# Kernel optimization log

Measured on AMD Instinct MI355X. Metric: run time of the kernel, lower is better.

The kernel has to match this reference:

```python
import jax, jax.numpy as jnp
import numpy as np

B, L, D = 8, 2048, 64


def setup_inputs() -> dict:
    key = jax.random.key(0)
    kq, kk, kv = jax.random.split(key, 3)
    query = jax.random.normal(kq, (B, L, D), dtype=jnp.float32)
    key_t = jax.random.normal(kk, (B, L, D), dtype=jnp.float32)
    value = jax.random.normal(kv, (B, L, D), dtype=jnp.float32)
    return {"query": query, "key": key_t, "value": value}


def reference(query, key, value):
    d = query.shape[-1]
    # e = Q K^T / sqrt(d_k)   -> [B, Lq, Lk]
    scale = 1.0 / np.sqrt(float(d)).astype(np.float32)
    e = jnp.einsum("bqd,bkd->bqk", query, key) * scale
    # stable softmax over keys (matches exp(e - max)/sum in source)
    attention = jax.nn.softmax(e, axis=-1)
    # v = A V   -> [B, Lq, Dv]
    return jnp.einsum("bqk,bkd->bqd", attention, value)
```

## Files before the change

### kernel.cpp

```cpp
#include <hip/hip_runtime.h>


#define B_ 8
#define L_ 2048
#define D_ 64
#define NT 256

typedef _Float16 half8_t __attribute__((ext_vector_type(8)));
typedef _Float16 half4_t __attribute__((ext_vector_type(4)));
typedef float f32x4 __attribute__((ext_vector_type(4)));

#define SCALE_LOG2E 0.1803368801111244f

__global__ __launch_bounds__(NT) void prepass_frag(
    const float* __restrict__ K, const float* __restrict__ V,
    _Float16* __restrict__ K16F, _Float16* __restrict__ VT16F)
{
    const int blk = blockIdx.x;
    const int t = threadIdx.x;
    if (blk < 512) {
        const int b  = blk >> 6;
        const int kt = blk & 63;
        const int p    = t >> 6;
        const int lane = t & 63;
        const int quad = lane >> 4;
        const int l15  = lane & 15;
        const int s = p >> 1, c = p & 1;
        const int row = kt * 32 + s * 16 + l15;
        const float* kp = K + ((size_t)b * L_ + row) * D_ + c * 32 + quad * 8;
        const float4 f0 = *(const float4*)kp;
        const float4 f1 = *(const float4*)(kp + 4);
        half8_t w;
        w[0] = (_Float16)f0.x; w[1] = (_Float16)f0.y;
        w[2] = (_Float16)f0.z; w[3] = (_Float16)f0.w;
        w[4] = (_Float16)f1.x; w[5] = (_Float16)f1.y;
        w[6] = (_Float16)f1.z; w[7] = (_Float16)f1.w;
        *(half8_t*)&K16F[((size_t)(b * 64 + kt) * 4 + p) * 512 + lane * 8] = w;
    } else {
        const int vb = blk - 512;
        const int b  = vb >> 6;
        const int kt = vb & 63;
        #pragma unroll
        for (int i = 0; i < 2; ++i) {
            const int slot = i * NT + t;
            const int p    = slot >> 6;
            const int lane = slot & 63;
            const int quad = lane >> 4;
            const int l15  = lane & 15;
            const int d = p >> 1, ks = p & 1;
            const int row = kt * 32 + ks * 16 + quad * 4;
            const int col = d * 16 + l15;
            const float* vp = V + ((size_t)b * L_ + row) * D_ + col;
            half4_t a;
            a[0] = (_Float16)vp[0];
            a[1] = (_Float16)vp[D_];
            a[2] = (_Float16)vp[2 * D_];
            a[3] = (_Float16)vp[3 * D_];
            *(half4_t*)&VT16F[((size_t)(b * 64 + kt) * 8 + p) * 256 + lane * 4] = a;
        }
    }
}


#define LOADK(KT, BK)                                                           \
    {                                                                           \
        _Pragma("unroll") for (int s = 0; s < 2; ++s)                           \
        _Pragma("unroll") for (int c = 0; c < 2; ++c)                           \
            BK[s][c] = *(const half8_t*)&KbF[((size_t)(KT) * 4 + s * 2 + c) * 512 + lane * 8]; \
    }

#define PROC(KT, BK)                                                            \
    {                                                                           \
        half4_t av[4][2];                                                       \
        _Pragma("unroll") for (int d = 0; d < 4; ++d)                           \
        _Pragma("unroll") for (int ks = 0; ks < 2; ++ks)                        \
            av[d][ks] = *(const half4_t*)&VbF[((size_t)(KT) * 8 + d * 2 + ks) * 256 + lane * 4]; \
        f32x4 sc[2][2];                                                         \
        _Pragma("unroll") for (int ks = 0; ks < 2; ++ks)                        \
        _Pragma("unroll") for (int qs = 0; qs < 2; ++qs) {                      \
            f32x4 acc = (f32x4){0.f, 0.f, 0.f, 0.f};                            \
            acc = __builtin_amdgcn_mfma_f32_16x16x32_f16(BK[ks][0], bq[qs][0], acc, 0, 0, 0); \
            acc = __builtin_amdgcn_mfma_f32_16x16x32_f16(BK[ks][1], bq[qs][1], acc, 0, 0, 0); \
            sc[ks][qs] = acc;                                                   \
        }                                                                       \
        half4_t pb[2][2];                                                       \
        _Pragma("unroll") for (int ks = 0; ks < 2; ++ks)                        \
        _Pragma("unroll") for (int qs = 0; qs < 2; ++qs) {                      \
            const float p0 = __builtin_exp2f(sc[ks][qs][0]);                    \
            const float p1 = __builtin_exp2f(sc[ks][qs][1]);                    \
            const float p2 = __builtin_exp2f(sc[ks][qs][2]);                    \
            const float p3 = __builtin_exp2f(sc[ks][qs][3]);                    \
            lacc[qs] += (p0 + p1) + (p2 + p3);                                  \
            half4_t pv;                                                         \
            pv[0] = (_Float16)p0; pv[1] = (_Float16)p1;                         \
            pv[2] = (_Float16)p2; pv[3] = (_Float16)p3;                         \
            pb[ks][qs] = pv;                                                    \
        }                                                                       \
        _Pragma("unroll") for (int qs = 0; qs < 2; ++qs)                        \
        _Pragma("unroll") for (int d = 0; d < 4; ++d)                           \
        _Pragma("unroll") for (int ks = 0; ks < 2; ++ks)                        \
            ofr[qs][d] = __builtin_amdgcn_mfma_f32_16x16x16f16(av[d][ks], pb[ks][qs], ofr[qs][d], 0, 0, 0); \
    }

__global__ __launch_bounds__(512, 4) void attn_tlp(
    const float* __restrict__ Q,
    const _Float16* __restrict__ K16F,
    const _Float16* __restrict__ VT16F,
    float* __restrict__ O)
{
    __shared__ float Ored[512 * 17];
    __shared__ float Lred[256];

    const int t    = threadIdx.x;
    const int wave = t >> 6;
    const int lane = t & 63;
    const int quad = lane >> 4;
    const int l15  = lane & 15;

    const int b   = blockIdx.x & 7;
    const int qbi = blockIdx.x >> 3;
    const int qb  = qbi * 32;
    const int kt0 = wave * 8;

    const _Float16* KbF = K16F + (size_t)b * 64 * 4 * 512;
    const _Float16* VbF = VT16F + (size_t)b * 64 * 8 * 256;

    half8_t bq[2][2];
    #pragma unroll
    for (int qs = 0; qs < 2; ++qs) {
        const float* qp = Q + ((size_t)b * L_ + qb + qs * 16 + l15) * D_ + quad * 8;
        #pragma unroll
        for (int c = 0; c < 2; ++c) {
            const float4 f0 = *(const float4*)(qp + c * 32);
            const float4 f1 = *(const float4*)(qp + c * 32 + 4);
            bq[qs][c][0] = (_Float16)(f0.x * SCALE_LOG2E);
            bq[qs][c][1] = (_Float16)(f0.y * SCALE_LOG2E);
            bq[qs][c][2] = (_Float16)(f0.z * SCALE_LOG2E);
            bq[qs][c][3] = (_Float16)(f0.w * SCALE_LOG2E);
            bq[qs][c][4] = (_Float16)(f1.x * SCALE_LOG2E);
            bq[qs][c][5] = (_Float16)(f1.y * SCALE_LOG2E);
            bq[qs][c][6] = (_Float16)(f1.z * SCALE_LOG2E);
            bq[qs][c][7] = (_Float16)(f1.w * SCALE_LOG2E);
        }
    }

    f32x4 ofr[2][4];
    #pragma unroll
    for (int qs = 0; qs < 2; ++qs)
        #pragma unroll
        for (int d = 0; d < 4; ++d)
            ofr[qs][d] = (f32x4){0.f, 0.f, 0.f, 0.f};
    float lacc[2] = {0.f, 0.f};

    half8_t bkA[2][2], bkB[2][2];
    LOADK(kt0, bkA);
    for (int it = 0; it < 4; ++it) {
        const int kta = kt0 + it * 2;
        LOADK(kta + 1, bkB);
        PROC(kta, bkA);
        LOADK(kta + 2, bkA);
        PROC(kta + 1, bkB);
    }

    #pragma unroll
    for (int qs = 0; qs < 2; ++qs) {
        float v = lacc[qs];
        v += __shfl_xor(v, 16, 64);
        v += __shfl_xor(v, 32, 64);
        lacc[qs] = v;
    }
    if (quad == 0) {
        Lred[wave * 32 + l15] = lacc[0];
        Lred[wave * 32 + 16 + l15] = lacc[1];
    }

    #pragma unroll
    for (int qs = 0; qs < 2; ++qs) {
        __syncthreads();
        #pragma unroll
        for (int d = 0; d < 4; ++d)
            #pragma unroll
            for (int r = 0; r < 4; ++r)
                Ored[(wave * 64 + lane) * 17 + d * 4 + r] = ofr[qs][d][r];
        __syncthreads();
        if (wave < 4) {
            float lt = 0.f;
            #pragma unroll
            for (int w2 = 0; w2 < 8; ++w2)
                lt += Lred[w2 * 32 + qs * 16 + l15];
            const float inv = 1.0f / lt;
            f32x4 osum = (f32x4){0.f, 0.f, 0.f, 0.f};
            #pragma unroll
            for (int w2 = 0; w2 < 8; ++w2) {
                const float* src = &Ored[(w2 * 64 + lane) * 17 + wave * 4];
                osum[0] += src[0]; osum[1] += src[1];
                osum[2] += src[2]; osum[3] += src[3];
            }
            float4 outv;
            outv.x = osum[0] * inv; outv.y = osum[1] * inv;
            outv.z = osum[2] * inv; outv.w = osum[3] * inv;
            *(float4*)&O[((size_t)b * L_ + qb + qs * 16 + l15) * D_ + wave * 16 + quad * 4] = outv;
        }
    }
}

#define KS 72
__global__ __launch_bounds__(NT) void attn_mfma_f16(
    const float* __restrict__ Q, const float* __restrict__ K,
    const float* __restrict__ V, float* __restrict__ O)
{
    __shared__ __align__(16) _Float16 Kt[64 * KS];
    __shared__ __align__(16) _Float16 Vt[D_ * KS];
    __shared__ __align__(16) _Float16 Pt[4][16 * KS];

    const int t = threadIdx.x;
    const int wave = t >> 6, lane = t & 63, quad = lane >> 4, l15 = lane & 15;
    const int bpb = L_ / 64;
    const int b = blockIdx.x / bpb;
    const int qb = (blockIdx.x % bpb) * 64 + wave * 16;
    const size_t boff = (size_t)b * L_ * D_;

    half8_t aq[2];
    {
        const float* qp = Q + boff + (size_t)(qb + l15) * D_ + quad * 8;
        #pragma unroll
        for (int c = 0; c < 2; ++c) {
            const float4* p4 = (const float4*)(qp + c * 32);
            const float4 f0 = p4[0], f1 = p4[1];
            aq[c][0] = (_Float16)f0.x; aq[c][1] = (_Float16)f0.y;
            aq[c][2] = (_Float16)f0.z; aq[c][3] = (_Float16)f0.w;
            aq[c][4] = (_Float16)f1.x; aq[c][5] = (_Float16)f1.y;
            aq[c][6] = (_Float16)f1.z; aq[c][7] = (_Float16)f1.w;
        }
    }
    f32x4 ofr[4];
    #pragma unroll
    for (int d = 0; d < 4; ++d) ofr[d] = (f32x4){0.f, 0.f, 0.f, 0.f};
    float lacc[4] = {0.f, 0.f, 0.f, 0.f};
    const int skey = t & 63, sdg = t >> 6;
    _Float16* Pw = &Pt[wave][0];

    for (int kt = 0; kt < L_ / 64; ++kt) {
        __syncthreads();
        {
            const float4* kg4 = (const float4*)(K + boff + (size_t)(kt * 64 + skey) * D_ + sdg * 16);
            const float4 f0 = kg4[0], f1 = kg4[1], f2 = kg4[2], f3 = kg4[3];
            half8_t w0, w1;
            w0[0] = (_Float16)f0.x; w0[1] = (_Float16)f0.y;
            w0[2] = (_Float16)f0.z; w0[3] = (_Float16)f0.w;
            w0[4] = (_Float16)f1.x; w0[5] = (_Float16)f1.y;
            w0[6] = (_Float16)f1.z; w0[7] = (_Float16)f1.w;
            w1[0] = (_Float16)f2.x; w1[1] = (_Float16)f2.y;
            w1[2] = (_Float16)f2.z; w1[3] = (_Float16)f2.w;
            w1[4] = (_Float16)f3.x; w1[5] = (_Float16)f3.y;
            w1[6] = (_Float16)f3.z; w1[7] = (_Float16)f3.w;
            *(half8_t*)&Kt[skey * KS + sdg * 16] = w0;
            *(half8_t*)&Kt[skey * KS + sdg * 16 + 8] = w1;
        }
        {
            const float4* vg4 = (const float4*)(V + boff + (size_t)(kt * 64 + skey) * D_ + sdg * 16);
            #pragma unroll
            for (int i = 0; i < 4; ++i) {
                const float4 f = vg4[i];
                const int d0 = sdg * 16 + i * 4;
                Vt[(d0 + 0) * KS + skey] = (_Float16)f.x;
                Vt[(d0 + 1) * KS + skey] = (_Float16)f.y;
                Vt[(d0 + 2) * KS + skey] = (_Float16)f.z;
                Vt[(d0 + 3) * KS + skey] = (_Float16)f.w;
            }
        }
        __syncthreads();
        #pragma unroll
        for (int s = 0; s < 4; ++s) {
            const half8_t bk0 = *(const half8_t*)&Kt[(s * 16 + l15) * KS + quad * 8];
            const half8_t bk1 = *(const half8_t*)&Kt[(s * 16 + l15) * KS + 32 + quad * 8];
            f32x4 sc = (f32x4){0.f, 0.f, 0.f, 0.f};
            sc = __builtin_amdgcn_mfma_f32_16x16x32_f16(aq[0], bk0, sc, 0, 0, 0);
            sc = __builtin_amdgcn_mfma_f32_16x16x32_f16(aq[1], bk1, sc, 0, 0, 0);
            #pragma unroll
            for (int r = 0; r < 4; ++r) {
                const float p = __expf(sc[r] * 0.125f);
                lacc[r] += p;
                Pw[(quad * 4 + r) * KS + s * 16 + l15] = (_Float16)p;
            }
        }
        __syncthreads();
        #pragma unroll
        for (int c = 0; c < 2; ++c) {
            const half8_t ap = *(const half8_t*)&Pw[l15 * KS + c * 32 + quad * 8];
            #pragma unroll
            for (int d = 0; d < 4; ++d) {
                const half8_t bv = *(const half8_t*)&Vt[(d * 16 + l15) * KS + c * 32 + quad * 8];
                ofr[d] = __builtin_amdgcn_mfma_f32_16x16x32_f16(ap, bv, ofr[d], 0, 0, 0);
            }
        }
    }
    #pragma unroll
    for (int r = 0; r < 4; ++r) {
        float v = lacc[r];
        v += __shfl_xor(v, 1, 64);
        v += __shfl_xor(v, 2, 64);
        v += __shfl_xor(v, 4, 64);
        v += __shfl_xor(v, 8, 64);
        lacc[r] = v;
    }
    #pragma unroll
    for (int r = 0; r < 4; ++r) {
        const float inv = 1.0f / lacc[r];
        float* orow = O + boff + (size_t)(qb + quad * 4 + r) * D_ + l15;
        #pragma unroll
        for (int d = 0; d < 4; ++d) orow[d * 16] = ofr[d][r] * inv;
    }
}

extern "C" void kernel_launch(void* const* d_in, const int* in_sizes, int n_in,
                              void* d_out, int out_size, void* d_ws, size_t ws_size,
                              hipStream_t stream) {
    const float* Q = (const float*)d_in[0];
    const float* K = (const float*)d_in[1];
    const float* V = (const float*)d_in[2];
    float* O = (float*)d_out;

    if (ws_size >= (size_t)8 * 1024 * 1024) {
        _Float16* K16F  = (_Float16*)d_ws;
        _Float16* VT16F = K16F + (size_t)1048576;
        prepass_frag<<<1024, NT, 0, stream>>>(K, V, K16F, VT16F);
        attn_tlp<<<512, 512, 0, stream>>>(Q, K16F, VT16F, O);
    } else {
        attn_mfma_f16<<<256, NT, 0, stream>>>(Q, K, V, O);
    }
}
```

Baseline: 83.33 us.

## Fuse K/V fp16 conversion into attention kernel with double-buffered LDS tiles

Drops the separate prepass kernel and its global fp16 workspace. A single fused kernel now loads fp32 K/V, converts them into MFMA fragment layout in double-buffered shared memory, and prefetches the next tile from global memory while computing the current one. Each block covers 64 queries with 8 waves, split into 4 query groups by 2 key halves, and the two halves are combined through LDS at the end. This removes one launch and the workspace round trip. In exchange there are fewer blocks (256), a barrier on every tile, and each block repeats the fp32-to-fp16 conversion work.

```diff
diff --git a/kernel.cpp b/kernel.cpp
--- a/kernel.cpp
+++ b/kernel.cpp
@@ -4,7 +4,6 @@
 #define B_ 8
 #define L_ 2048
 #define D_ 64
-#define NT 256
 
 typedef _Float16 half8_t __attribute__((ext_vector_type(8)));
 typedef _Float16 half4_t __attribute__((ext_vector_type(4)));
@@ -12,304 +11,173 @@
 
 #define SCALE_LOG2E 0.1803368801111244f
 
-__global__ __launch_bounds__(NT) void prepass_frag(
-    const float* __restrict__ K, const float* __restrict__ V,
-    _Float16* __restrict__ K16F, _Float16* __restrict__ VT16F)
+__global__ __launch_bounds__(512, 2) void attn_fused(
+    const float* __restrict__ Q, const float* __restrict__ K,
+    const float* __restrict__ V, float* __restrict__ O)
 {
-    const int blk = blockIdx.x;
-    const int t = threadIdx.x;
-    if (blk < 512) {
-        const int b  = blk >> 6;
-        const int kt = blk & 63;
-        const int p    = t >> 6;
-        const int lane = t & 63;
-        const int quad = lane >> 4;
-        const int l15  = lane & 15;
-        const int s = p >> 1, c = p & 1;
-        const int row = kt * 32 + s * 16 + l15;
-        const float* kp = K + ((size_t)b * L_ + row) * D_ + c * 32 + quad * 8;
-        const float4 f0 = *(const float4*)kp;
-        const float4 f1 = *(const float4*)(kp + 4);
-        half8_t w;
-        w[0] = (_Float16)f0.x; w[1] = (_Float16)f0.y;
-        w[2] = (_Float16)f0.z; w[3] = (_Float16)f0.w;
-        w[4] = (_Float16)f1.x; w[5] = (_Float16)f1.y;
-        w[6] = (_Float16)f1.z; w[7] = (_Float16)f1.w;
-        *(half8_t*)&K16F[((size_t)(b * 64 + kt) * 4 + p) * 512 + lane * 8] = w;
-    } else {
-        const int vb = blk - 512;
-        const int b  = vb >> 6;
-        const int kt = vb & 63;
-        #pragma unroll
-        for (int i = 0; i < 2; ++i) {
-            const int slot = i * NT + t;
-            const int p    = slot >> 6;
-            const int lane = slot & 63;
-            const int quad = lane >> 4;
-            const int l15  = lane & 15;
-            const int d = p >> 1, ks = p & 1;
-            const int row = kt * 32 + ks * 16 + quad * 4;
-            const int col = d * 16 + l15;
-            const float* vp = V + ((size_t)b * L_ + row) * D_ + col;
-            half4_t a;
-            a[0] = (_Float16)vp[0];
-            a[1] = (_Float16)vp[D_];
-            a[2] = (_Float16)vp[2 * D_];
-            a[3] = (_Float16)vp[3 * D_];
-            *(half4_t*)&VT16F[((size_t)(b * 64 + kt) * 8 + p) * 256 + lane * 4] = a;
-        }
-    }
-}
-
-
-#define LOADK(KT, BK)                                                           \
-    {                                                                           \
-        _Pragma("unroll") for (int s = 0; s < 2; ++s)                           \
-        _Pragma("unroll") for (int c = 0; c < 2; ++c)                           \
-            BK[s][c] = *(const half8_t*)&KbF[((size_t)(KT) * 4 + s * 2 + c) * 512 + lane * 8]; \
-    }
-
-#define PROC(KT, BK)                                                            \
-    {                                                                           \
-        half4_t av[4][2];                                                       \
-        _Pragma("unroll") for (int d = 0; d < 4; ++d)                           \
-        _Pragma("unroll") for (int ks = 0; ks < 2; ++ks)                        \
-            av[d][ks] = *(const half4_t*)&VbF[((size_t)(KT) * 8 + d * 2 + ks) * 256 + lane * 4]; \
-        f32x4 sc[2][2];                                                         \
-        _Pragma("unroll") for (int ks = 0; ks < 2; ++ks)                        \
-        _Pragma("unroll") for (int qs = 0; qs < 2; ++qs) {                      \
-            f32x4 acc = (f32x4){0.f, 0.f, 0.f, 0.f};                            \
-            acc = __builtin_amdgcn_mfma_f32_16x16x32_f16(BK[ks][0], bq[qs][0], acc, 0, 0, 0); \
-            acc = __builtin_amdgcn_mfma_f32_16x16x32_f16(BK[ks][1], bq[qs][1], acc, 0, 0, 0); \
-            sc[ks][qs] = acc;                                                   \
-        }                                                                       \
-        half4_t pb[2][2];                                                       \
-        _Pragma("unroll") for (int ks = 0; ks < 2; ++ks)                        \
-        _Pragma("unroll") for (int qs = 0; qs < 2; ++qs) {                      \
-            const float p0 = __builtin_exp2f(sc[ks][qs][0]);                    \
-            const float p1 = __builtin_exp2f(sc[ks][qs][1]);                    \
-            const float p2 = __builtin_exp2f(sc[ks][qs][2]);                    \
-            const float p3 = __builtin_exp2f(sc[ks][qs][3]);                    \
-            lacc[qs] += (p0 + p1) + (p2 + p3);                                  \
-            half4_t pv;                                                         \
-            pv[0] = (_Float16)p0; pv[1] = (_Float16)p1;                         \
-            pv[2] = (_Float16)p2; pv[3] = (_Float16)p3;                         \
-            pb[ks][qs] = pv;                                                    \
-        }                                                                       \
-        _Pragma("unroll") for (int qs = 0; qs < 2; ++qs)                        \
-        _Pragma("unroll") for (int d = 0; d < 4; ++d)                           \
-        _Pragma("unroll") for (int ks = 0; ks < 2; ++ks)                        \
-            ofr[qs][d] = __builtin_amdgcn_mfma_f32_16x16x16f16(av[d][ks], pb[ks][qs], ofr[qs][d], 0, 0, 0); \
-    }
-
-__global__ __launch_bounds__(512, 4) void attn_tlp(
-    const float* __restrict__ Q,
-    const _Float16* __restrict__ K16F,
-    const _Float16* __restrict__ VT16F,
-    float* __restrict__ O)
-{
-    __shared__ float Ored[512 * 17];
-    __shared__ float Lred[256];
+    __shared__ __align__(16) _Float16 FR[16384];
 
     const int t    = threadIdx.x;
     const int wave = t >> 6;
     const int lane = t & 63;
     const int quad = lane >> 4;
     const int l15  = lane & 15;
+    const int qg   = wave & 3;
+    const int kg   = wave >> 2;
 
     const int b   = blockIdx.x & 7;
     const int qbi = blockIdx.x >> 3;
-    const int qb  = qbi * 32;
-    const int kt0 = wave * 8;
+    const int qb  = qbi * 64;
 
-    const _Float16* KbF = K16F + (size_t)b * 64 * 4 * 512;
-    const _Float16* VbF = VT16F + (size_t)b * 64 * 8 * 256;
+    const size_t boff = (size_t)b * L_ * D_;
 
-    half8_t bq[2][2];
+    const int skg = t >> 8;
+    const int kj  = t & 255;
+    const int kp    = kj >> 6, kjl = kj & 63;
+    const int kquad = kjl >> 4, kl15 = kjl & 15;
+    const int ks_ = kp >> 1, kc = kp & 1;
+    const int ksrc0 = (ks_ * 16 + kl15) * D_ + kc * 32 + kquad * 8;
+    const int kldst = skg * 4096 + kp * 512 + kjl * 8;
+
+    int vsrc0[2], vldst[2];
     #pragma unroll
-    for (int qs = 0; qs < 2; ++qs) {
-        const float* qp = Q + ((size_t)b * L_ + qb + qs * 16 + l15) * D_ + quad * 8;
+    for (int i = 0; i < 2; ++i) {
+        const int j  = (t & 255) * 2 + i;
+        const int p  = j >> 6, jl = j & 63;
+        const int vq = jl >> 4, vl = jl & 15;
+        const int d  = p >> 1, vks = p & 1;
+        vsrc0[i] = (vks * 16 + vq * 4) * D_ + d * 16 + vl;
+        vldst[i] = skg * 4096 + 2048 + p * 256 + jl * 4;
+    }
+    const int tile0 = skg * 32;
+
+    half8_t bq[2];
+    {
+        const float* qp = Q + boff + (size_t)(qb + qg * 16 + l15) * D_ + quad * 8;
         #pragma unroll
         for (int c = 0; c < 2; ++c) {
             const float4 f0 = *(const float4*)(qp + c * 32);
             const float4 f1 = *(const float4*)(qp + c * 32 + 4);
-            bq[qs][c][0] = (_Float16)(f0.x * SCALE_LOG2E);
-            bq[qs][c][1] = (_Float16)(f0.y * SCALE_LOG2E);
-            bq[qs][c][2] = (_Float16)(f0.z * SCALE_LOG2E);
-            bq[qs][c][3] = (_Float16)(f0.w * SCALE_LOG2E);
-            bq[qs][c][4] = (_Float16)(f1.x * SCALE_LOG2E);
-            bq[qs][c][5] = (_Float16)(f1.y * SCALE_LOG2E);
-            bq[qs][c][6] = (_Float16)(f1.z * SCALE_LOG2E);
-            bq[qs][c][7] = (_Float16)(f1.w * SCALE_LOG2E);
+            bq[c][0] = (_Float16)(f0.x * SCALE_LOG2E);
+            bq[c][1] = (_Float16)(f0.y * SCALE_LOG2E);
+            bq[c][2] = (_Float16)(f0.z * SCALE_LOG2E);
+            bq[c][3] = (_Float16)(f0.w * SCALE_LOG2E);
+            bq[c][4] = (_Float16)(f1.x * SCALE_LOG2E);
+            bq[c][5] = (_Float16)(f1.y * SCALE_LOG2E);
+            bq[c][6] = (_Float16)(f1.z * SCALE_LOG2E);
+            bq[c][7] = (_Float16)(f1.w * SCALE_LOG2E);
         }
     }
 
-    f32x4 ofr[2][4];
+    f32x4 ofr[4];
     #pragma unroll
-    for (int qs = 0; qs < 2; ++qs)
-        #pragma unroll
-        for (int d = 0; d < 4; ++d)
-            ofr[qs][d] = (f32x4){0.f, 0.f, 0.f, 0.f};
-    float lacc[2] = {0.f, 0.f};
+    for (int d = 0; d < 4; ++d) ofr[d] = (f32x4){0.f, 0.f, 0.f, 0.f};
+    float lacc = 0.f;
 
-    half8_t bkA[2][2], bkB[2][2];
-    LOADK(kt0, bkA);
-    for (int it = 0; it < 4; ++it) {
-        const int kta = kt0 + it * 2;
-        LOADK(kta + 1, bkB);
-        PROC(kta, bkA);
-        LOADK(kta + 2, bkA);
-        PROC(kta + 1, bkB);
+    float4 kf0, kf1;
+    float  vf[2][4];
+
+#define GLOAD(TT)                                                              \
+    {                                                                          \
+        const float* kpp = K + boff + (size_t)(tile0 + (TT)) * 32 * D_ + ksrc0;\
+        kf0 = *(const float4*)kpp;                                             \
+        kf1 = *(const float4*)(kpp + 4);                                       \
+        _Pragma("unroll") for (int i = 0; i < 2; ++i) {                        \
+            const float* vpp =                                                 \
+                V + boff + (size_t)(tile0 + (TT)) * 32 * D_ + vsrc0[i];        \
+            vf[i][0] = vpp[0];      vf[i][1] = vpp[D_];                        \
+            vf[i][2] = vpp[2 * D_]; vf[i][3] = vpp[3 * D_];                    \
+        }                                                                      \
     }
 
-    #pragma unroll
-    for (int qs = 0; qs < 2; ++qs) {
-        float v = lacc[qs];
-        v += __shfl_xor(v, 16, 64);
-        v += __shfl_xor(v, 32, 64);
-        lacc[qs] = v;
-    }
-    if (quad == 0) {
-        Lred[wave * 32 + l15] = lacc[0];
-        Lred[wave * 32 + 16 + l15] = lacc[1];
+#define SWRITE(BUF)                                                            \
+    {                                                                          \
+        half8_t w;                                                             \
+        w[0] = (_Float16)kf0.x; w[1] = (_Float16)kf0.y;                        \
+        w[2] = (_Float16)kf0.z; w[3] = (_Float16)kf0.w;                        \
+        w[4] = (_Float16)kf1.x; w[5] = (_Float16)kf1.y;                        \
+        w[6] = (_Float16)kf1.z; w[7] = (_Float16)kf1.w;                        \
+        *(half8_t*)&FR[(BUF) * 8192 + kldst] = w;                              \
+        _Pragma("unroll") for (int i = 0; i < 2; ++i) {                        \
+            half4_t a;                                                         \
+            a[0] = (_Float16)vf[i][0]; a[1] = (_Float16)vf[i][1];              \
+            a[2] = (_Float16)vf[i][2]; a[3] = (_Float16)vf[i][3];              \
+            *(half4_t*)&FR[(BUF) * 8192 + vldst[i]] = a;                       \
+        }                                                                      \
     }
 
-    #pragma unroll
-    for (int qs = 0; qs < 2; ++qs) {
-        __syncthreads();
+    GLOAD(0);
+    SWRITE(0);
+    GLOAD(1);
+    __syncthreads();
+
+    const _Float16* Kb = &FR[kg * 4096];
+    const _Float16* Vb = Kb + 2048;
+
+    for (int tt = 0; tt < 32; ++tt) {
+        const int cb = (tt & 1) * 8192;
+        if (tt < 31) {
+            SWRITE((tt & 1) ^ 1);
+            if (tt < 30) GLOAD(tt + 2);
+        }
+        half8_t bk[2][2];
+        #pragma unroll
+        for (int s = 0; s < 2; ++s)
+            #pragma unroll
+            for (int c = 0; c < 2; ++c)
+                bk[s][c] = *(const half8_t*)&Kb[cb + (s * 2 + c) * 512 + lane * 8];
+        half4_t av[4][2];
         #pragma unroll
         for (int d = 0; d < 4; ++d)
             #pragma unroll
-            for (int r = 0; r < 4; ++r)
-                Ored[(wave * 64 + lane) * 17 + d * 4 + r] = ofr[qs][d][r];
-        __syncthreads();
-        if (wave < 4) {
-            float lt = 0.f;
+            for (int ks = 0; ks < 2; ++ks)
+                av[d][ks] = *(const half4_t*)&Vb[cb + (d * 2 + ks) * 256 + lane * 4];
+        #pragma unroll
+        for (int ks = 0; ks < 2; ++ks) {
+            f32x4 acc = (f32x4){0.f, 0.f, 0.f, 0.f};
+            acc = __builtin_amdgcn_mfma_f32_16x16x32_f16(bk[ks][0], bq[0], acc, 0, 0, 0);
+            acc = __builtin_amdgcn_mfma_f32_16x16x32_f16(bk[ks][1], bq[1], acc, 0, 0, 0);
+            const float p0 = __builtin_exp2f(acc[0]);
+            const float p1 = __builtin_exp2f(acc[1]);
+            const float p2 = __builtin_exp2f(acc[2]);
+            const float p3 = __builtin_exp2f(acc[3]);
+            lacc += (p0 + p1) + (p2 + p3);
+            half4_t pv;
+            pv[0] = (_Float16)p0; pv[1] = (_Float16)p1;
+            pv[2] = (_Float16)p2; pv[3] = (_Float16)p3;
             #pragma unroll
-            for (int w2 = 0; w2 < 8; ++w2)
-                lt += Lred[w2 * 32 + qs * 16 + l15];
-            const float inv = 1.0f / lt;
-            f32x4 osum = (f32x4){0.f, 0.f, 0.f, 0.f};
-            #pragma unroll
-            for (int w2 = 0; w2 < 8; ++w2) {
-                const float* src = &Ored[(w2 * 64 + lane) * 17 + wave * 4];
-                osum[0] += src[0]; osum[1] += src[1];
-                osum[2] += src[2]; osum[3] += src[3];
-            }
-            float4 outv;
-            outv.x = osum[0] * inv; outv.y = osum[1] * inv;
-            outv.z = osum[2] * inv; outv.w = osum[3] * inv;
-            *(float4*)&O[((size_t)b * L_ + qb + qs * 16 + l15) * D_ + wave * 16 + quad * 4] = outv;
-        }
-    }
-}
-
-#define KS 72
-__global__ __launch_bounds__(NT) void attn_mfma_f16(
-    const float* __restrict__ Q, const float* __restrict__ K,
-    const float* __restrict__ V, float* __restrict__ O)
-{
-    __shared__ __align__(16) _Float16 Kt[64 * KS];
-    __shared__ __align__(16) _Float16 Vt[D_ * KS];
-    __shared__ __align__(16) _Float16 Pt[4][16 * KS];
-
-    const int t = threadIdx.x;
-    const int wave = t >> 6, lane = t & 63, quad = lane >> 4, l15 = lane & 15;
-    const int bpb = L_ / 64;
-    const int b = blockIdx.x / bpb;
-    const int qb = (blockIdx.x % bpb) * 64 + wave * 16;
-    const size_t boff = (size_t)b * L_ * D_;
-
-    half8_t aq[2];
-    {
-        const float* qp = Q + boff + (size_t)(qb + l15) * D_ + quad * 8;
-        #pragma unroll
-        for (int c = 0; c < 2; ++c) {
-            const float4* p4 = (const float4*)(qp + c * 32);
-            const float4 f0 = p4[0], f1 = p4[1];
-            aq[c][0] = (_Float16)f0.x; aq[c][1] = (_Float16)f0.y;
-            aq[c][2] = (_Float16)f0.z; aq[c][3] = (_Float16)f0.w;
-            aq[c][4] = (_Float16)f1.x; aq[c][5] = (_Float16)f1.y;
-            aq[c][6] = (_Float16)f1.z; aq[c][7] = (_Float16)f1.w;
-        }
-    }
-    f32x4 ofr[4];
-    #pragma unroll
-    for (int d = 0; d < 4; ++d) ofr[d] = (f32x4){0.f, 0.f, 0.f, 0.f};
-    float lacc[4] = {0.f, 0.f, 0.f, 0.f};
-    const int skey = t & 63, sdg = t >> 6;
-    _Float16* Pw = &Pt[wave][0];
-
-    for (int kt = 0; kt < L_ / 64; ++kt) {
-        __syncthreads();
-        {
-            const float4* kg4 = (const float4*)(K + boff + (size_t)(kt * 64 + skey) * D_ + sdg * 16);
-            const float4 f0 = kg4[0], f1 = kg4[1], f2 = kg4[2], f3 = kg4[3];
-            half8_t w0, w1;
-            w0[0] = (_Float16)f0.x; w0[1] = (_Float16)f0.y;
-            w0[2] = (_Float16)f0.z; w0[3] = (_Float16)f0.w;
-            w0[4] = (_Float16)f1.x; w0[5] = (_Float16)f1.y;
-            w0[6] = (_Float16)f1.z; w0[7] = (_Float16)f1.w;
-            w1[0] = (_Float16)f2.x; w1[1] = (_Float16)f2.y;
-            w1[2] = (_Float16)f2.z; w1[3] = (_Float16)f2.w;
-            w1[4] = (_Float16)f3.x; w1[5] = (_Float16)f3.y;
-            w1[6] = (_Float16)f3.z; w1[7] = (_Float16)f3.w;
-            *(half8_t*)&Kt[skey * KS + sdg * 16] = w0;
-            *(half8_t*)&Kt[skey * KS + sdg * 16 + 8] = w1;
-        }
-        {
-            const float4* vg4 = (const float4*)(V + boff + (size_t)(kt * 64 + skey) * D_ + sdg * 16);
-            #pragma unroll
-            for (int i = 0; i < 4; ++i) {
-                const float4 f = vg4[i];
-                const int d0 = sdg * 16 + i * 4;
-                Vt[(d0 + 0) * KS + skey] = (_Float16)f.x;
-                Vt[(d0 + 1) * KS + skey] = (_Float16)f.y;
-                Vt[(d0 + 2) * KS + skey] = (_Float16)f.z;
-                Vt[(d0 + 3) * KS + skey] = (_Float16)f.w;
-            }
+            for (int d = 0; d < 4; ++d)
+                ofr[d] = __builtin_amdgcn_mfma_f32_16x16x16f16(av[d][ks], pv, ofr[d], 0, 0, 0);
         }
         __syncthreads();
+    }
+
+    float lsum = lacc;
+    lsum += __shfl_xor(lsum, 16, 64);
+    lsum += __shfl_xor(lsum, 32, 64);
+
+    float* red = (float*)&FR[0];
+    if (kg == 1) {
+        float* dst = red + (qg * 64 + lane) * 17;
         #pragma unroll
-        for (int s = 0; s < 4; ++s) {
-            const half8_t bk0 = *(const half8_t*)&Kt[(s * 16 + l15) * KS + quad * 8];
-            const half8_t bk1 = *(const half8_t*)&Kt[(s * 16 + l15) * KS + 32 + quad * 8];
-            f32x4 sc = (f32x4){0.f, 0.f, 0.f, 0.f};
-            sc = __builtin_amdgcn_mfma_f32_16x16x32_f16(aq[0], bk0, sc, 0, 0, 0);
-            sc = __builtin_amdgcn_mfma_f32_16x16x32_f16(aq[1], bk1, sc, 0, 0, 0);
+        for (int d = 0; d < 4; ++d)
             #pragma unroll
-            for (int r = 0; r < 4; ++r) {
-                const float p = __expf(sc[r] * 0.125f);
-                lacc[r] += p;
-                Pw[(quad * 4 + r) * KS + s * 16 + l15] = (_Float16)p;
-            }
+            for (int r = 0; r < 4; ++r) dst[d * 4 + r] = ofr[d][r];
+        dst[16] = lsum;
+    }
+    __syncthreads();
+    if (kg == 0) {
+        const float* src = red + (qg * 64 + lane) * 17;
+        const float inv = 1.0f / (lsum + src[16]);
+        #pragma unroll
+        for (int d = 0; d < 4; ++d) {
+            float4 o;
+            o.x = (ofr[d][0] + src[d * 4 + 0]) * inv;
+            o.y = (ofr[d][1] + src[d * 4 + 1]) * inv;
+            o.z = (ofr[d][2] + src[d * 4 + 2]) * inv;
+            o.w = (ofr[d][3] + src[d * 4 + 3]) * inv;
+            *(float4*)&O[boff + (size_t)(qb + qg * 16 + l15) * D_ + d * 16 + quad * 4] = o;
         }
-        __syncthreads();
-        #pragma unroll
-        for (int c = 0; c < 2; ++c) {
-            const half8_t ap = *(const half8_t*)&Pw[l15 * KS + c * 32 + quad * 8];
-            #pragma unroll
-            for (int d = 0; d < 4; ++d) {
-                const half8_t bv = *(const half8_t*)&Vt[(d * 16 + l15) * KS + c * 32 + quad * 8];
-                ofr[d] = __builtin_amdgcn_mfma_f32_16x16x32_f16(ap, bv, ofr[d], 0, 0, 0);
-            }
-        }
-    }
-    #pragma unroll
-    for (int r = 0; r < 4; ++r) {
-        float v = lacc[r];
-        v += __shfl_xor(v, 1, 64);
-        v += __shfl_xor(v, 2, 64);
-        v += __shfl_xor(v, 4, 64);
-        v += __shfl_xor(v, 8, 64);
-        lacc[r] = v;
-    }
-    #pragma unroll
-    for (int r = 0; r < 4; ++r) {
-        const float inv = 1.0f / lacc[r];
-        float* orow = O + boff + (size_t)(qb + quad * 4 + r) * D_ + l15;
-        #pragma unroll
-        for (int d = 0; d < 4; ++d) orow[d * 16] = ofr[d][r] * inv;
     }
 }
 
@@ -320,13 +188,6 @@
     const float* K = (const float*)d_in[1];
     const float* V = (const float*)d_in[2];
     float* O = (float*)d_out;
-
-    if (ws_size >= (size_t)8 * 1024 * 1024) {
-        _Float16* K16F  = (_Float16*)d_ws;
-        _Float16* VT16F = K16F + (size_t)1048576;
-        prepass_frag<<<1024, NT, 0, stream>>>(K, V, K16F, VT16F);
-        attn_tlp<<<512, 512, 0, stream>>>(Q, K16F, VT16F, O);
-    } else {
-        attn_mfma_f16<<<256, NT, 0, stream>>>(Q, K, V, O);
-    }
+    (void)d_ws; (void)ws_size;
+    attn_fused<<<256, 512, 0, stream>>>(Q, K, V, O);
 }
```

Result: slower. 92.34 us (+10.8%).

## Replace prepass+tlp with split-K attention staging K/V tiles in LDS plus combine kernel

Applied to the files above, without the earlier changes.

Drops the separate K/V fp16 conversion prepass. Each block now converts a 256-key slice of K and V into LDS once and reuses it across 256 queries handled by 8 waves. Per-split partial outputs and row sums go to a workspace and a second combine kernel reduces them. The aim is to avoid the extra prepass launch and the repeated global fragment reads. In exchange it writes and reads a 32 MB fp32 partial buffer and needs a larger workspace, so it may fall back to the slow path if the workspace is too small.

```diff
diff --git a/kernel.cpp b/kernel.cpp
--- a/kernel.cpp
+++ b/kernel.cpp
@@ -4,7 +4,6 @@
 #define B_ 8
 #define L_ 2048
 #define D_ 64
-#define NT 256
 
 typedef _Float16 half8_t __attribute__((ext_vector_type(8)));
 typedef _Float16 half4_t __attribute__((ext_vector_type(4)));
@@ -12,104 +11,13 @@
 
 #define SCALE_LOG2E 0.1803368801111244f
 
-__global__ __launch_bounds__(NT) void prepass_frag(
-    const float* __restrict__ K, const float* __restrict__ V,
-    _Float16* __restrict__ K16F, _Float16* __restrict__ VT16F)
+__global__ __launch_bounds__(512, 4) void attn_splitk(
+    const float* __restrict__ Q, const float* __restrict__ K,
+    const float* __restrict__ V, float* __restrict__ PW,
+    float* __restrict__ LW)
 {
-    const int blk = blockIdx.x;
-    const int t = threadIdx.x;
-    if (blk < 512) {
-        const int b  = blk >> 6;
-        const int kt = blk & 63;
-        const int p    = t >> 6;
-        const int lane = t & 63;
-        const int quad = lane >> 4;
-        const int l15  = lane & 15;
-        const int s = p >> 1, c = p & 1;
-        const int row = kt * 32 + s * 16 + l15;
-        const float* kp = K + ((size_t)b * L_ + row) * D_ + c * 32 + quad * 8;
-        const float4 f0 = *(const float4*)kp;
-        const float4 f1 = *(const float4*)(kp + 4);
-        half8_t w;
-        w[0] = (_Float16)f0.x; w[1] = (_Float16)f0.y;
-        w[2] = (_Float16)f0.z; w[3] = (_Float16)f0.w;
-        w[4] = (_Float16)f1.x; w[5] = (_Float16)f1.y;
-        w[6] = (_Float16)f1.z; w[7] = (_Float16)f1.w;
-        *(half8_t*)&K16F[((size_t)(b * 64 + kt) * 4 + p) * 512 + lane * 8] = w;
-    } else {
-        const int vb = blk - 512;
-        const int b  = vb >> 6;
-        const int kt = vb & 63;
-        #pragma unroll
-        for (int i = 0; i < 2; ++i) {
-            const int slot = i * NT + t;
-            const int p    = slot >> 6;
-            const int lane = slot & 63;
-            const int quad = lane >> 4;
-            const int l15  = lane & 15;
-            const int d = p >> 1, ks = p & 1;
-            const int row = kt * 32 + ks * 16 + quad * 4;
-            const int col = d * 16 + l15;
-            const float* vp = V + ((size_t)b * L_ + row) * D_ + col;
-            half4_t a;
-            a[0] = (_Float16)vp[0];
-            a[1] = (_Float16)vp[D_];
-            a[2] = (_Float16)vp[2 * D_];
-            a[3] = (_Float16)vp[3 * D_];
-            *(half4_t*)&VT16F[((size_t)(b * 64 + kt) * 8 + p) * 256 + lane * 4] = a;
-        }
-    }
-}
-
-
-#define LOADK(KT, BK)                                                           \
-    {                                                                           \
-        _Pragma("unroll") for (int s = 0; s < 2; ++s)                           \
-        _Pragma("unroll") for (int c = 0; c < 2; ++c)                           \
-            BK[s][c] = *(const half8_t*)&KbF[((size_t)(KT) * 4 + s * 2 + c) * 512 + lane * 8]; \
-    }
-
-#define PROC(KT, BK)                                                            \
-    {                                                                           \
-        half4_t av[4][2];                                                       \
-        _Pragma("unroll") for (int d = 0; d < 4; ++d)                           \
-        _Pragma("unroll") for (int ks = 0; ks < 2; ++ks)                        \
-            av[d][ks] = *(const half4_t*)&VbF[((size_t)(KT) * 8 + d * 2 + ks) * 256 + lane * 4]; \
-        f32x4 sc[2][2];                                                         \
-        _Pragma("unroll") for (int ks = 0; ks < 2; ++ks)                        \
-        _Pragma("unroll") for (int qs = 0; qs < 2; ++qs) {                      \
-            f32x4 acc = (f32x4){0.f, 0.f, 0.f, 0.f};                            \
-            acc = __builtin_amdgcn_mfma_f32_16x16x32_f16(BK[ks][0], bq[qs][0], acc, 0, 0, 0); \
-            acc = __builtin_amdgcn_mfma_f32_16x16x32_f16(BK[ks][1], bq[qs][1], acc, 0, 0, 0); \
-            sc[ks][qs] = acc;                                                   \
-        }                                                                       \
-        half4_t pb[2][2];                                                       \
-        _Pragma("unroll") for (int ks = 0; ks < 2; ++ks)                        \
-        _Pragma("unroll") for (int qs = 0; qs < 2; ++qs) {                      \
-            const float p0 = __builtin_exp2f(sc[ks][qs][0]);                    \
-            const float p1 = __builtin_exp2f(sc[ks][qs][1]);                    \
-            const float p2 = __builtin_exp2f(sc[ks][qs][2]);                    \
-            const float p3 = __builtin_exp2f(sc[ks][qs][3]);                    \
-            lacc[qs] += (p0 + p1) + (p2 + p3);                                  \
-            half4_t pv;                                                         \
-            pv[0] = (_Float16)p0; pv[1] = (_Float16)p1;                         \
-            pv[2] = (_Float16)p2; pv[3] = (_Float16)p3;                         \
-            pb[ks][qs] = pv;                                                    \
-        }                                                                       \
-        _Pragma("unroll") for (int qs = 0; qs < 2; ++qs)                        \
-        _Pragma("unroll") for (int d = 0; d < 4; ++d)                           \
-        _Pragma("unroll") for (int ks = 0; ks < 2; ++ks)                        \
-            ofr[qs][d] = __builtin_amdgcn_mfma_f32_16x16x16f16(av[d][ks], pb[ks][qs], ofr[qs][d], 0, 0, 0); \
-    }
-
-__global__ __launch_bounds__(512, 4) void attn_tlp(
-    const float* __restrict__ Q,
-    const _Float16* __restrict__ K16F,
-    const _Float16* __restrict__ VT16F,
-    float* __restrict__ O)
-{
-    __shared__ float Ored[512 * 17];
-    __shared__ float Lred[256];
+    __shared__ __align__(16) _Float16 KL[16384];
+    __shared__ __align__(16) _Float16 VL[16384];
 
     const int t    = threadIdx.x;
     const int wave = t >> 6;
@@ -117,18 +25,19 @@
     const int quad = lane >> 4;
     const int l15  = lane & 15;
 
-    const int b   = blockIdx.x & 7;
-    const int qbi = blockIdx.x >> 3;
-    const int qb  = qbi * 32;
-    const int kt0 = wave * 8;
-
-    const _Float16* KbF = K16F + (size_t)b * 64 * 4 * 512;
-    const _Float16* VbF = VT16F + (size_t)b * 64 * 8 * 256;
+    const int blk = blockIdx.x;
+    const int b   = blk & 7;
+    const int kg  = (blk >> 3) & 7;
+    const int qc  = blk >> 6;
+
+    const size_t boff = (size_t)b * L_ * D_;
+    const int key0 = kg * 256;
+    const int q0   = qc * 256 + wave * 32;
 
     half8_t bq[2][2];
     #pragma unroll
     for (int qs = 0; qs < 2; ++qs) {
-        const float* qp = Q + ((size_t)b * L_ + qb + qs * 16 + l15) * D_ + quad * 8;
+        const float* qp = Q + boff + (size_t)(q0 + qs * 16 + l15) * D_ + quad * 8;
         #pragma unroll
         for (int c = 0; c < 2; ++c) {
             const float4 f0 = *(const float4*)(qp + c * 32);
@@ -144,6 +53,42 @@
         }
     }
 
+    #pragma unroll
+    for (int i = 0; i < 4; ++i) {
+        const int j  = i * 512 + t;
+        const int kt = j >> 8, kj = j & 255;
+        const int p  = kj >> 6, jl = kj & 63;
+        const int jq = jl >> 4, jl15 = jl & 15;
+        const int s = p >> 1, c = p & 1;
+        const int row = key0 + kt * 32 + s * 16 + jl15;
+        const float* kp = K + boff + (size_t)row * D_ + c * 32 + jq * 8;
+        const float4 f0 = *(const float4*)kp;
+        const float4 f1 = *(const float4*)(kp + 4);
+        half8_t w;
+        w[0] = (_Float16)f0.x; w[1] = (_Float16)f0.y;
+        w[2] = (_Float16)f0.z; w[3] = (_Float16)f0.w;
+        w[4] = (_Float16)f1.x; w[5] = (_Float16)f1.y;
+        w[6] = (_Float16)f1.z; w[7] = (_Float16)f1.w;
+        *(half8_t*)&KL[kt * 2048 + p * 512 + jl * 8] = w;
+    }
+    #pragma unroll
+    for (int i = 0; i < 8; ++i) {
+        const int j  = i * 512 + t;
+        const int kt = j >> 9, kj = j & 511;
+        const int p  = kj >> 6, jl = kj & 63;
+        const int jq = jl >> 4, jl15 = jl & 15;
+        const int d = p >> 1, ks = p & 1;
+        const int row = key0 + kt * 32 + ks * 16 + jq * 4;
+        const float* vp = V + boff + (size_t)row * D_ + d * 16 + jl15;
+        half4_t a;
+        a[0] = (_Float16)vp[0];
+        a[1] = (_Float16)vp[D_];
+        a[2] = (_Float16)vp[2 * D_];
+        a[3] = (_Float16)vp[3 * D_];
+        *(half4_t*)&VL[kt * 2048 + d * 512 + jl * 8 + ks * 4] = a;
+    }
+    __syncthreads();
+
     f32x4 ofr[2][4];
     #pragma unroll
     for (int qs = 0; qs < 2; ++qs)
@@ -152,58 +97,94 @@
             ofr[qs][d] = (f32x4){0.f, 0.f, 0.f, 0.f};
     float lacc[2] = {0.f, 0.f};
 
-    half8_t bkA[2][2], bkB[2][2];
-    LOADK(kt0, bkA);
-    for (int it = 0; it < 4; ++it) {
-        const int kta = kt0 + it * 2;
-        LOADK(kta + 1, bkB);
-        PROC(kta, bkA);
-        LOADK(kta + 2, bkA);
-        PROC(kta + 1, bkB);
-    }
-
+    #pragma unroll
+    for (int kt = 0; kt < 8; ++kt) {
+        const _Float16* Kt = &KL[kt * 2048];
+        const _Float16* Vt = &VL[kt * 2048];
+        half8_t bk[2][2];
+        #pragma unroll
+        for (int s = 0; s < 2; ++s)
+            #pragma unroll
+            for (int c = 0; c < 2; ++c)
+                bk[s][c] = *(const half8_t*)&Kt[(s * 2 + c) * 512 + lane * 8];
+        half4_t pv[2][2];
+        #pragma unroll
+        for (int ks = 0; ks < 2; ++ks)
+            #pragma unroll
+            for (int qs = 0; qs < 2; ++qs) {
+                f32x4 acc = (f32x4){0.f, 0.f, 0.f, 0.f};
+                acc = __builtin_amdgcn_mfma_f32_16x16x32_f16(bk[ks][0], bq[qs][0], acc, 0, 0, 0);
+                acc = __builtin_amdgcn_mfma_f32_16x16x32_f16(bk[ks][1], bq[qs][1], acc, 0, 0, 0);
+                const float p0 = __builtin_exp2f(acc[0]);
+                const float p1 = __builtin_exp2f(acc[1]);
+                const float p2 = __builtin_exp2f(acc[2]);
+                const float p3 = __builtin_exp2f(acc[3]);
+                lacc[qs] += (p0 + p1) + (p2 + p3);
+                half4_t pw;
+                pw[0] = (_Float16)p0; pw[1] = (_Float16)p1;
+                pw[2] = (_Float16)p2; pw[3] = (_Float16)p3;
+                pv[ks][qs] = pw;
+            }
+        #pragma unroll
+        for (int d = 0; d < 4; ++d) {
+            const half8_t av8 = *(const half8_t*)&Vt[d * 512 + lane * 8];
+            const half4_t alo = __builtin_shufflevector(av8, av8, 0, 1, 2, 3);
+            const half4_t ahi = __builtin_shufflevector(av8, av8, 4, 5, 6, 7);
+            #pragma unroll
+            for (int qs = 0; qs < 2; ++qs) {
+                ofr[qs][d] = __builtin_amdgcn_mfma_f32_16x16x16f16(alo, pv[0][qs], ofr[qs][d], 0, 0, 0);
+                ofr[qs][d] = __builtin_amdgcn_mfma_f32_16x16x16f16(ahi, pv[1][qs], ofr[qs][d], 0, 0, 0);
+            }
+        }
+    }
+
+    const size_t pbase = (size_t)(b * 8 + kg) * L_;
     #pragma unroll
     for (int qs = 0; qs < 2; ++qs) {
         float v = lacc[qs];
         v += __shfl_xor(v, 16, 64);
         v += __shfl_xor(v, 32, 64);
-        lacc[qs] = v;
-    }
-    if (quad == 0) {
-        Lred[wave * 32 + l15] = lacc[0];
-        Lred[wave * 32 + 16 + l15] = lacc[1];
-    }
-
-    #pragma unroll
-    for (int qs = 0; qs < 2; ++qs) {
-        __syncthreads();
-        #pragma unroll
-        for (int d = 0; d < 4; ++d)
-            #pragma unroll
-            for (int r = 0; r < 4; ++r)
-                Ored[(wave * 64 + lane) * 17 + d * 4 + r] = ofr[qs][d][r];
-        __syncthreads();
-        if (wave < 4) {
-            float lt = 0.f;
-            #pragma unroll
-            for (int w2 = 0; w2 < 8; ++w2)
-                lt += Lred[w2 * 32 + qs * 16 + l15];
-            const float inv = 1.0f / lt;
-            f32x4 osum = (f32x4){0.f, 0.f, 0.f, 0.f};
-            #pragma unroll
-            for (int w2 = 0; w2 < 8; ++w2) {
-                const float* src = &Ored[(w2 * 64 + lane) * 17 + wave * 4];
-                osum[0] += src[0]; osum[1] += src[1];
-                osum[2] += src[2]; osum[3] += src[3];
-            }
-            float4 outv;
-            outv.x = osum[0] * inv; outv.y = osum[1] * inv;
-            outv.z = osum[2] * inv; outv.w = osum[3] * inv;
-            *(float4*)&O[((size_t)b * L_ + qb + qs * 16 + l15) * D_ + wave * 16 + quad * 4] = outv;
-        }
+        const int q = q0 + qs * 16 + l15;
+        float* pw = PW + (pbase + q) * D_;
+        #pragma unroll
+        for (int d = 0; d < 4; ++d) {
+            float4 o;
+            o.x = ofr[qs][d][0]; o.y = ofr[qs][d][1];
+            o.z = ofr[qs][d][2]; o.w = ofr[qs][d][3];
+            *(float4*)&pw[d * 16 + quad * 4] = o;
+        }
+        if (quad == 0) LW[pbase + q] = v;
     }
 }
 
+__global__ __launch_bounds__(256) void combine(
+    const float* __restrict__ PW, const float* __restrict__ LW,
+    float* __restrict__ O)
+{
+    const int blk = blockIdx.x;
+    const int b  = blk & 7;
+    const int qi = blk >> 3;
+    const int t  = threadIdx.x;
+    const int lq = t >> 4;
+    const int c4 = t & 15;
+    const int q  = qi * 16 + lq;
+
+    f32x4 s = (f32x4){0.f, 0.f, 0.f, 0.f};
+    float l = 0.f;
+    #pragma unroll
+    for (int kg = 0; kg < 8; ++kg) {
+        const size_t pbase = (size_t)(b * 8 + kg) * L_ + q;
+        const float4 pv = *(const float4*)&PW[pbase * D_ + c4 * 4];
+        s[0] += pv.x; s[1] += pv.y; s[2] += pv.z; s[3] += pv.w;
+        l += LW[pbase];
+    }
+    const float inv = 1.0f / l;
+    float4 o;
+    o.x = s[0] * inv; o.y = s[1] * inv; o.z = s[2] * inv; o.w = s[3] * inv;
+    *(float4*)&O[((size_t)b * L_ + q) * D_ + c4 * 4] = o;
+}
+
+#define NT 256
 #define KS 72
 __global__ __launch_bounds__(NT) void attn_mfma_f16(
     const float* __restrict__ Q, const float* __restrict__ K,
@@ -321,11 +302,13 @@
     const float* V = (const float*)d_in[2];
     float* O = (float*)d_out;
 
-    if (ws_size >= (size_t)8 * 1024 * 1024) {
-        _Float16* K16F  = (_Float16*)d_ws;
-        _Float16* VT16F = K16F + (size_t)1048576;
-        prepass_frag<<<1024, NT, 0, stream>>>(K, V, K16F, VT16F);
-        attn_tlp<<<512, 512, 0, stream>>>(Q, K16F, VT16F, O);
+    const size_t pw_elts = (size_t)B_ * 8 * L_ * D_;
+    const size_t need = pw_elts * 4 + (size_t)B_ * 8 * L_ * 4;
+    if (ws_size >= need) {
+        float* PW = (float*)d_ws;
+        float* LW = PW + pw_elts;
+        attn_splitk<<<512, 512, 0, stream>>>(Q, K, V, PW, LW);
+        combine<<<1024, 256, 0, stream>>>(PW, LW, O);
     } else {
         attn_mfma_f16<<<256, NT, 0, stream>>>(Q, K, V, O);
     }
```

Result: slower. 101.9 us (+22.3%).

## Process 64 queries per block to double K/V fragment reuse, prefetch V

Applied to the files above, without the earlier changes.

The main attention kernel now covers 64 query rows per block instead of 32, so each K/V fragment loaded from global memory feeds twice as many MFMAs, and the grid is halved to 256 blocks. V fragments are now double-buffered and prefetched alongside K instead of being loaded inside the compute step. The prepass block index mapping is interleaved by batch, and an unused modulo wrap is added to the tile index. Costs are higher register pressure (occupancy hint lowered to 2), a longer output reduction, and only 256 blocks on the device.

```diff
diff --git a/kernel.cpp b/kernel.cpp
--- a/kernel.cpp
+++ b/kernel.cpp
@@ -19,8 +19,8 @@
     const int blk = blockIdx.x;
     const int t = threadIdx.x;
     if (blk < 512) {
-        const int b  = blk >> 6;
-        const int kt = blk & 63;
+        const int b  = blk & 7;
+        const int kt = blk >> 3;
         const int p    = t >> 6;
         const int lane = t & 63;
         const int quad = lane >> 4;
@@ -38,8 +38,8 @@
         *(half8_t*)&K16F[((size_t)(b * 64 + kt) * 4 + p) * 512 + lane * 8] = w;
     } else {
         const int vb = blk - 512;
-        const int b  = vb >> 6;
-        const int kt = vb & 63;
+        const int b  = vb & 7;
+        const int kt = vb >> 3;
         #pragma unroll
         for (int i = 0; i < 2; ++i) {
             const int slot = i * NT + t;
@@ -64,52 +64,52 @@
 
 #define LOADK(KT, BK)                                                           \
     {                                                                           \
+        const int ktc_ = (KT) & 63;                                             \
         _Pragma("unroll") for (int s = 0; s < 2; ++s)                           \
         _Pragma("unroll") for (int c = 0; c < 2; ++c)                           \
-            BK[s][c] = *(const half8_t*)&KbF[((size_t)(KT) * 4 + s * 2 + c) * 512 + lane * 8]; \
-    }
-
-#define PROC(KT, BK)                                                            \
+            BK[s][c] = *(const half8_t*)&KbF[((size_t)ktc_ * 4 + s * 2 + c) * 512 + lane * 8]; \
+    }
+
+#define LOADV(KT, AV)                                                           \
     {                                                                           \
-        half4_t av[4][2];                                                       \
+        const int ktc_ = (KT) & 63;                                             \
         _Pragma("unroll") for (int d = 0; d < 4; ++d)                           \
         _Pragma("unroll") for (int ks = 0; ks < 2; ++ks)                        \
-            av[d][ks] = *(const half4_t*)&VbF[((size_t)(KT) * 8 + d * 2 + ks) * 256 + lane * 4]; \
-        f32x4 sc[2][2];                                                         \
+            AV[d][ks] = *(const half4_t*)&VbF[((size_t)ktc_ * 8 + d * 2 + ks) * 256 + lane * 4]; \
+    }
+
+#define PROC(BK, AV)                                                            \
+    {                                                                           \
+        half4_t pb[2][4];                                                       \
         _Pragma("unroll") for (int ks = 0; ks < 2; ++ks)                        \
-        _Pragma("unroll") for (int qs = 0; qs < 2; ++qs) {                      \
+        _Pragma("unroll") for (int qf = 0; qf < 4; ++qf) {                      \
             f32x4 acc = (f32x4){0.f, 0.f, 0.f, 0.f};                            \
-            acc = __builtin_amdgcn_mfma_f32_16x16x32_f16(BK[ks][0], bq[qs][0], acc, 0, 0, 0); \
-            acc = __builtin_amdgcn_mfma_f32_16x16x32_f16(BK[ks][1], bq[qs][1], acc, 0, 0, 0); \
-            sc[ks][qs] = acc;                                                   \
-        }                                                                       \
-        half4_t pb[2][2];                                                       \
-        _Pragma("unroll") for (int ks = 0; ks < 2; ++ks)                        \
-        _Pragma("unroll") for (int qs = 0; qs < 2; ++qs) {                      \
-            const float p0 = __builtin_exp2f(sc[ks][qs][0]);                    \
-            const float p1 = __builtin_exp2f(sc[ks][qs][1]);                    \
-            const float p2 = __builtin_exp2f(sc[ks][qs][2]);                    \
-            const float p3 = __builtin_exp2f(sc[ks][qs][3]);                    \
-            lacc[qs] += (p0 + p1) + (p2 + p3);                                  \
+            acc = __builtin_amdgcn_mfma_f32_16x16x32_f16(BK[ks][0], bq[qf][0], acc, 0, 0, 0); \
+            acc = __builtin_amdgcn_mfma_f32_16x16x32_f16(BK[ks][1], bq[qf][1], acc, 0, 0, 0); \
+            const float p0 = __builtin_exp2f(acc[0]);                           \
+            const float p1 = __builtin_exp2f(acc[1]);                           \
+            const float p2 = __builtin_exp2f(acc[2]);                           \
+            const float p3 = __builtin_exp2f(acc[3]);                           \
+            lacc[qf] += (p0 + p1) + (p2 + p3);                                  \
             half4_t pv;                                                         \
             pv[0] = (_Float16)p0; pv[1] = (_Float16)p1;                         \
             pv[2] = (_Float16)p2; pv[3] = (_Float16)p3;                         \
-            pb[ks][qs] = pv;                                                    \
+            pb[ks][qf] = pv;                                                    \
         }                                                                       \
-        _Pragma("unroll") for (int qs = 0; qs < 2; ++qs)                        \
+        _Pragma("unroll") for (int qf = 0; qf < 4; ++qf)                        \
         _Pragma("unroll") for (int d = 0; d < 4; ++d)                           \
         _Pragma("unroll") for (int ks = 0; ks < 2; ++ks)                        \
-            ofr[qs][d] = __builtin_amdgcn_mfma_f32_16x16x16f16(av[d][ks], pb[ks][qs], ofr[qs][d], 0, 0, 0); \
-    }
-
-__global__ __launch_bounds__(512, 4) void attn_tlp(
+            ofr[qf][d] = __builtin_amdgcn_mfma_f32_16x16x16f16(AV[d][ks], pb[ks][qf], ofr[qf][d], 0, 0, 0); \
+    }
+
+__global__ __launch_bounds__(512, 2) void attn_q64(
     const float* __restrict__ Q,
     const _Float16* __restrict__ K16F,
     const _Float16* __restrict__ VT16F,
     float* __restrict__ O)
 {
     __shared__ float Ored[512 * 17];
-    __shared__ float Lred[256];
+    __shared__ float Lred[512];
 
     const int t    = threadIdx.x;
     const int wave = t >> 6;
@@ -119,75 +119,81 @@
 
     const int b   = blockIdx.x & 7;
     const int qbi = blockIdx.x >> 3;
-    const int qb  = qbi * 32;
+    const int qb  = qbi * 64;
     const int kt0 = wave * 8;
 
     const _Float16* KbF = K16F + (size_t)b * 64 * 4 * 512;
     const _Float16* VbF = VT16F + (size_t)b * 64 * 8 * 256;
 
-    half8_t bq[2][2];
-    #pragma unroll
-    for (int qs = 0; qs < 2; ++qs) {
-        const float* qp = Q + ((size_t)b * L_ + qb + qs * 16 + l15) * D_ + quad * 8;
+    half8_t bq[4][2];
+    #pragma unroll
+    for (int qf = 0; qf < 4; ++qf) {
+        const float* qp = Q + ((size_t)b * L_ + qb + qf * 16 + l15) * D_ + quad * 8;
         #pragma unroll
         for (int c = 0; c < 2; ++c) {
             const float4 f0 = *(const float4*)(qp + c * 32);
             const float4 f1 = *(const float4*)(qp + c * 32 + 4);
-            bq[qs][c][0] = (_Float16)(f0.x * SCALE_LOG2E);
-            bq[qs][c][1] = (_Float16)(f0.y * SCALE_LOG2E);
-            bq[qs][c][2] = (_Float16)(f0.z * SCALE_LOG2E);
-            bq[qs][c][3] = (_Float16)(f0.w * SCALE_LOG2E);
-            bq[qs][c][4] = (_Float16)(f1.x * SCALE_LOG2E);
-            bq[qs][c][5] = (_Float16)(f1.y * SCALE_LOG2E);
-            bq[qs][c][6] = (_Float16)(f1.z * SCALE_LOG2E);
-            bq[qs][c][7] = (_Float16)(f1.w * SCALE_LOG2E);
-        }
-    }
-
-    f32x4 ofr[2][4];
-    #pragma unroll
-    for (int qs = 0; qs < 2; ++qs)
+            bq[qf][c][0] = (_Float16)(f0.x * SCALE_LOG2E);
+            bq[qf][c][1] = (_Float16)(f0.y * SCALE_LOG2E);
+            bq[qf][c][2] = (_Float16)(f0.z * SCALE_LOG2E);
+            bq[qf][c][3] = (_Float16)(f0.w * SCALE_LOG2E);
+            bq[qf][c][4] = (_Float16)(f1.x * SCALE_LOG2E);
+            bq[qf][c][5] = (_Float16)(f1.y * SCALE_LOG2E);
+            bq[qf][c][6] = (_Float16)(f1.z * SCALE_LOG2E);
+            bq[qf][c][7] = (_Float16)(f1.w * SCALE_LOG2E);
+        }
+    }
+
+    f32x4 ofr[4][4];
+    #pragma unroll
+    for (int qf = 0; qf < 4; ++qf)
         #pragma unroll
         for (int d = 0; d < 4; ++d)
-            ofr[qs][d] = (f32x4){0.f, 0.f, 0.f, 0.f};
-    float lacc[2] = {0.f, 0.f};
+            ofr[qf][d] = (f32x4){0.f, 0.f, 0.f, 0.f};
+    float lacc[4] = {0.f, 0.f, 0.f, 0.f};
 
     half8_t bkA[2][2], bkB[2][2];
+    half4_t avA[4][2], avB[4][2];
     LOADK(kt0, bkA);
+    LOADV(kt0, avA);
     for (int it = 0; it < 4; ++it) {
         const int kta = kt0 + it * 2;
         LOADK(kta + 1, bkB);
-        PROC(kta, bkA);
+        LOADV(kta + 1, avB);
+        PROC(bkA, avA);
         LOADK(kta + 2, bkA);
-        PROC(kta + 1, bkB);
-    }
-
-    #pragma unroll
-    for (int qs = 0; qs < 2; ++qs) {
-        float v = lacc[qs];
+        LOADV(kta + 2, avA);
+        PROC(bkB, avB);
+    }
+
+    #pragma unroll
+    for (int qf = 0; qf < 4; ++qf) {
+        float v = lacc[qf];
         v += __shfl_xor(v, 16, 64);
         v += __shfl_xor(v, 32, 64);
-        lacc[qs] = v;
+        lacc[qf] = v;
     }
     if (quad == 0) {
-        Lred[wave * 32 + l15] = lacc[0];
-        Lred[wave * 32 + 16 + l15] = lacc[1];
-    }
-
-    #pragma unroll
-    for (int qs = 0; qs < 2; ++qs) {
-        __syncthreads();
+        #pragma unroll
+        for (int qf = 0; qf < 4; ++qf)
+            Lred[wave * 64 + qf * 16 + l15] = lacc[qf];
+    }
+
+    #pragma unroll
+    for (int qf = 0; qf < 4; ++qf) {
+        __syncthreads();
+        float* dst = &Ored[(wave * 64 + lane) * 17];
         #pragma unroll
         for (int d = 0; d < 4; ++d)
             #pragma unroll
             for (int r = 0; r < 4; ++r)
-                Ored[(wave * 64 + lane) * 17 + d * 4 + r] = ofr[qs][d][r];
+                dst[d * 4 + r] = ofr[qf][d][r];
         __syncthreads();
         if (wave < 4) {
             float lt = 0.f;
             #pragma unroll
             for (int w2 = 0; w2 < 8; ++w2)
-                lt += Lred[w2 * 32 + qs * 16 + l15];
+                lt += Lred[w2 * 64 + qf * 16 + l15];
             const float inv = 1.0f / lt;
             f32x4 osum = (f32x4){0.f, 0.f, 0.f, 0.f};
             #pragma unroll
@@ -199,7 +205,7 @@
             float4 outv;
             outv.x = osum[0] * inv; outv.y = osum[1] * inv;
             outv.z = osum[2] * inv; outv.w = osum[3] * inv;
-            *(float4*)&O[((size_t)b * L_ + qb + qs * 16 + l15) * D_ + wave * 16 + quad * 4] = outv;
+            *(float4*)&O[((size_t)b * L_ + qb + qf * 16 + l15) * D_ + wave * 16 + quad * 4] = outv;
         }
     }
 }
@@ -325,7 +331,7 @@
         _Float16* K16F  = (_Float16*)d_ws;
         _Float16* VT16F = K16F + (size_t)1048576;
         prepass_frag<<<1024, NT, 0, stream>>>(K, V, K16F, VT16F);
-        attn_tlp<<<512, 512, 0, stream>>>(Q, K16F, VT16F, O);
+        attn_q64<<<256, 512, 0, stream>>>(Q, K16F, VT16F, O);
     } else {
         attn_mfma_f16<<<256, NT, 0, stream>>>(Q, K, V, O);
     }
```

After: 87.27 us. +4.7%, slower.
